# Kernel tuning notes

Measured on AMD Instinct MI355X. Metric: run time of the kernel, lower is better.

Reference implementation:

```python
import jax, jax.numpy as jnp
from jax import lax
import numpy as np

EPS = 1e-5  # BatchNorm2d default eps

def _cbs(x, w, g, b, m, v, pad):
    # Conv2d(bias=False) + BatchNorm2d (eval mode, running stats) + SiLU
    y = lax.conv_general_dilated(x, w, (1, 1), [(pad, pad), (pad, pad)],
                                 dimension_numbers=('NCHW', 'OIHW', 'NCHW'))
    y = (y - m[None, :, None, None]) * (g / jnp.sqrt(v + EPS))[None, :, None, None] + b[None, :, None, None]
    return y * jax.nn.sigmoid(y)

def setup_inputs():
    key = jax.random.key(0)
    B, C1, C2, H, W = 2, 128, 128, 20, 20
    ks = iter(jax.random.split(key, 16))
    def wconv(o, i, s):
        return jax.random.normal(next(ks), (o, i, s, s), jnp.float32) / np.float32(np.sqrt(i * s * s))
    def bn(cdim):
        k1, k2 = jax.random.split(next(ks))
        g = jax.random.uniform(k1, (cdim,), jnp.float32, 0.5, 1.5)
        b = jax.random.normal(k2, (cdim,), jnp.float32) * 0.1
        return g, b, jnp.zeros((cdim,), jnp.float32), jnp.ones((cdim,), jnp.float32)
    inp = {'x': jax.random.normal(next(ks), (B, C1, H, W), jnp.float32)}
    inp['w1'] = wconv(C2, C1, 1); inp['g1'], inp['b1'], inp['m1'], inp['v1'] = bn(C2)
    inp['w2'] = wconv(C2, C1, 1); inp['g2'], inp['b2'], inp['m2'], inp['v2'] = bn(C2)
    inp['wr1'] = wconv(C2, 2 * C2, 1); inp['gr1'], inp['br1'], inp['mr1'], inp['vr1'] = bn(C2)
    inp['wr2'] = wconv(C2, C2, 3); inp['gr2'], inp['br2'], inp['mr2'], inp['vr2'] = bn(C2)
    inp['wr3'] = wconv(1, C2, 1); inp['gr3'], inp['br3'], inp['mr3'], inp['vr3'] = bn(1)
    return inp

def reference(x, w1, g1, b1, m1, v1, w2, g2, b2, m2, v2,
              wr1, gr1, br1, mr1, vr1, wr2, gr2, br2, mr2, vr2,
              wr3, gr3, br3, mr3, vr3):
    B, C, H, W = x.shape
    HW = H * W
    # feat: [B, HW, C2]
    feat = _cbs(x, w1, g1, b1, m1, v1, 0).reshape(B, -1, HW).transpose(0, 2, 1)
    C2 = feat.shape[-1]
    # pairwise concat: rel[b,i,j] = [feat[b,i], feat[b,j]]  -> [B, HW, HW, 2*C2]
    fi = jnp.broadcast_to(feat[:, :, None, :], (B, HW, HW, C2))
    fj = jnp.broadcast_to(feat[:, None, :, :], (B, HW, HW, C2))
    rel = jnp.concatenate([fi, fj], axis=-1)
    # faithful permute(0,3,1,2) + contiguous view to [B*HW, 2*C2, H, W]
    rel = rel.transpose(0, 3, 1, 2).reshape(B * HW, 2 * C2, H, W)
    r = _cbs(rel, wr1, gr1, br1, mr1, vr1, 0)
    r = _cbs(r, wr2, gr2, br2, mr2, vr2, 1)
    r = _cbs(r, wr3, gr3, br3, mr3, vr3, 0)  # [B*HW, 1, H, W]
    scores = r.reshape(B, HW, HW)
    # bmm aggregation then back to [B, C2, H, W]
    att = jnp.einsum('bij,bjc->bic', scores, feat).transpose(0, 2, 1).reshape(B, C2, H, W)
    return _cbs(att, w2, g2, b2, m2, v2, 0) + x
```

## Files before the change

kernel.cpp:

```cpp
#include <hip/hip_runtime.h>

#define EPS 1e-5f

typedef __bf16 bf16x8 __attribute__((ext_vector_type(8)));
typedef float  f32x4  __attribute__((ext_vector_type(4)));

__device__ __forceinline__ unsigned short f2bf(float f) {
  unsigned int u = __float_as_uint(f);
  unsigned int r = (u + 0x7fffu + ((u >> 16) & 1u)) >> 16;
  return (unsigned short)r;
}
__device__ __forceinline__ float silu(float y) {
  return y * __builtin_amdgcn_rcpf(1.f + __expf(-y));
}

__global__ void prep_kernel(const float* __restrict__ x, const float* __restrict__ w1,
                            const float* __restrict__ g1, const float* __restrict__ b1,
                            const float* __restrict__ m1, const float* __restrict__ v1,
                            const float* __restrict__ wr2, const float* __restrict__ wr1,
                            const float* __restrict__ w2,
                            float* __restrict__ feat, float* __restrict__ featT,
                            float* __restrict__ attz,
                            unsigned short* __restrict__ Apack, float* __restrict__ Pfx,
                            float* __restrict__ Wt, float* __restrict__ W2t,
                            float* __restrict__ wr1T) {
  int blk = blockIdx.x;
  int tid = threadIdx.x;
  if (blk < 400) {
    int hp = tid >> 7, c = tid & 127;
    int pp = blk * 2 + hp;
    int b = pp / 400, p = pp % 400;
    __shared__ float xv[2][128];
    xv[hp][c] = x[(b * 128 + c) * 400 + p];
    __syncthreads();
    const float4* w4 = (const float4*)(w1 + c * 128);
    const float4* v4 = (const float4*)xv[hp];
    float s0 = 0.f, s1 = 0.f, s2 = 0.f, s3 = 0.f;
#pragma unroll
    for (int i = 0; i < 32; ++i) {
      float4 wv = w4[i], xx = v4[i];
      s0 += wv.x * xx.x; s1 += wv.y * xx.y; s2 += wv.z * xx.z; s3 += wv.w * xx.w;
    }
    float s = (s0 + s1) + (s2 + s3);
    float sc = g1[c] * rsqrtf(v1[c] + EPS);
    float y = s * sc + (b1[c] - m1[c] * sc);
    float f = silu(y);
    feat[(b * 400 + p) * 128 + c] = f;
    featT[(b * 128 + c) * 400 + p] = f;
    if (p >= 200) attz[(b * 400 + p) * 128 + c] = 0.f;
  } else if (blk < 472) {
    int f = (blk - 400) * 4 + (tid >> 6);
    int lane = tid & 63;
    int tap = f >> 5, ks = (f >> 3) & 3, m8 = f & 7;
    int o  = m8 * 16 + (lane & 15);
    int cb = ks * 32 + (lane >> 4) * 8;
    unsigned short* dst = Apack + ((size_t)f * 64 + lane) * 8;
#pragma unroll
    for (int j = 0; j < 8; ++j)
      dst[j] = f2bf(wr2[(o * 128 + (cb + j)) * 9 + tap]);
  } else if (blk < 504) {
    int o = (blk - 472) * 4 + (tid >> 6);
    int lane = tid & 63;
    float4 wv = ((const float4*)(wr1 + o * 256))[lane];
    float p0 = wv.x, p1 = p0 + wv.y, p2 = p1 + wv.z, p3 = p2 + wv.w;
    float v = p3;
#pragma unroll
    for (int d = 1; d < 64; d <<= 1) {
      float t = __shfl_up(v, d);
      if (lane >= d) v += t;
    }
    float off = v - p3;
    float* Po = Pfx + o * 257;
    if (lane == 0) Po[0] = 0.f;
    Po[lane * 4 + 1] = off + p0;
    Po[lane * 4 + 2] = off + p1;
    Po[lane * 4 + 3] = off + p2;
    Po[lane * 4 + 4] = off + p3;
  } else if (blk < 648) {
    int base = (blk - 504) * 1024;
#pragma unroll
    for (int k = 0; k < 4; ++k) {
      int idx = base + k * 256 + tid;
      int tap = idx >> 14;
      int r = idx & 16383;
      int i = r >> 7, o = r & 127;
      Wt[idx] = wr2[(o * 128 + i) * 9 + tap];
    }
  } else if (blk < 712) {
    int idx = (blk - 648) * 256 + tid;
    int i = idx >> 7, o = idx & 127;
    W2t[idx] = w2[o * 128 + i];
  } else {
    int base = (blk - 712) * 1024;
#pragma unroll
    for (int k = 0; k < 4; ++k) {
      int idx = base + k * 256 + tid;
      int i = idx >> 7, o = idx & 127;
      wr1T[idx] = wr1[o * 256 + i];
    }
  }
}

__global__ __launch_bounds__(512, 4) void rel_kernel(
    const float* __restrict__ feat, const float* __restrict__ featT,
    const float* __restrict__ wr1T, const float* __restrict__ Pfx,
    const float* __restrict__ gr1, const float* __restrict__ br1,
    const float* __restrict__ mr1, const float* __restrict__ vr1,
    const unsigned short* __restrict__ Apack, const float* __restrict__ Wt,
    const float* __restrict__ gr2, const float* __restrict__ br2,
    const float* __restrict__ mr2, const float* __restrict__ vr2,
    const float* __restrict__ wr3,
    const float* __restrict__ gr3, const float* __restrict__ br3,
    const float* __restrict__ mr3, const float* __restrict__ vr3,
    float* __restrict__ att) {

  __shared__ __align__(16) unsigned short r1f[16 * 221 * 8];
  __shared__ float f0s[220], f1s[220], scoreS[208];
  __shared__ float wB0s[128], wB1s[128];
  __shared__ float sc1[128], sh1[128], sc2[128], sh2[128], w3c[128];
  __shared__ float attT[128];
  __shared__ float fA[256], r1c[128], AvS[128];
  __shared__ float vS[9 * 128];
  __shared__ float spS[9];
  __shared__ float spP[400];

  int tid = threadIdx.x, lane = tid & 63, wid = tid >> 6;
  int blk = blockIdx.x;

  if (tid < 128) {
    float s1 = gr1[tid] * rsqrtf(vr1[tid] + EPS); sc1[tid] = s1; sh1[tid] = br1[tid] - mr1[tid] * s1;
    float s2 = gr2[tid] * rsqrtf(vr2[tid] + EPS); sc2[tid] = s2; sh2[tid] = br2[tid] - mr2[tid] * s2;
    w3c[tid] = wr3[tid];
    attT[tid] = 0.f; AvS[tid] = 0.f;
  }
  float s3 = gr3[0] * rsqrtf(vr3[0] + EPS);
  float sh3 = br3[0] - mr3[0] * s3;

  if (blk < 800) {
    int idx = blk >> 1, half = blk & 1;
    int b = idx / 200, q = 200 + idx % 200;
    int c0 = (q * 256) / 400, c1 = c0 + 1;
    if (tid < 128) {
      const float* Po = Pfx + tid * 257;
      int e0 = min(256, 400 * c0 + 400 - 256 * q);
      wB0s[tid] = Po[e0];
      float wv = 0.f;
      if (c1 < 256) {
        int s1i = min(256, max(0, 400 * c1 - 256 * q));
        wv = Po[256] - Po[s1i];
      }
      wB1s[tid] = wv;
    }
    if (tid < 220) {
      int p = tid + 180 * half;
      f0s[tid] = featT[(b * 128 + (c0 - 128)) * 400 + p];
      f1s[tid] = (c1 < 256) ? featT[(b * 128 + (c1 - 128)) * 400 + p] : 0.f;
    }
    if (tid < 208) scoreS[tid] = 0.f;
    __syncthreads();

    for (int i = tid; i < 3520; i += 512) {
      int plane = i / 220, p = i - plane * 220;
      int cb = (plane >> 2) * 32 + (plane & 3) * 8;
      float fa0 = f0s[p], fa1 = f1s[p];
      unsigned int pk[4];
#pragma unroll
      for (int jp = 0; jp < 4; ++jp) {
        int c = cb + jp * 2;
        float y0 = wB0s[c] * fa0 + wB1s[c] * fa1;     y0 = y0 * sc1[c] + sh1[c];
        float y1 = wB0s[c + 1] * fa0 + wB1s[c + 1] * fa1; y1 = y1 * sc1[c + 1] + sh1[c + 1];
        pk[jp] = (unsigned int)f2bf(silu(y0)) | ((unsigned int)f2bf(silu(y1)) << 16);
      }
      *(uint4*)&r1f[(plane * 221 + p) * 8] = make_uint4(pk[0], pk[1], pk[2], pk[3]);
    }
    if (tid < 16) *(uint4*)&r1f[(tid * 221 + 220) * 8] = make_uint4(0, 0, 0, 0);

    int wm = wid & 1, wn = wid >> 1;
    int ntcnt = (wn == 0) ? 4 : 3;
    int n16 = lane & 15, quad = lane >> 4;
    int hA[4], wA[4], poA[4]; bool pov[4];
#pragma unroll
    for (int t = 0; t < 4; ++t) {
      int po = (wn + 4 * t) * 16 + n16;
      poA[t] = po; pov[t] = po < 200;
      int pg = half * 200 + po;
      hA[t] = pg / 20; wA[t] = pg - 20 * hA[t];
    }
    f32x4 acc[4][4];
#pragma unroll
    for (int mt = 0; mt < 4; ++mt)
#pragma unroll
      for (int t = 0; t < 4; ++t) acc[mt][t] = f32x4{0.f, 0.f, 0.f, 0.f};

    __syncthreads();

    const char* wbase = (const char*)Apack + (size_t)((wm * 4) * 64 + lane) * 16;
    for (int tap = 0; tap < 9; ++tap) {
      int dy = tap / 3 - 1, dx = tap % 3 - 1;
      int pp[4];
#pragma unroll
      for (int t = 0; t < 4; ++t) {
        int hh = hA[t] + dy, ww = wA[t] + dx;
        bool valid = pov[t] & (hh >= 0) & (hh < 20) & (ww >= 0) & (ww < 20);
        pp[t] = valid ? (hh - 9 * half) * 20 + ww : 220;
      }
#pragma unroll
      for (int ks = 0; ks < 4; ++ks) {
        const char* wp = wbase + (size_t)(tap * 4 + ks) * 8192;
        bf16x8 af0 = *(const bf16x8*)(wp);
        bf16x8 af1 = *(const bf16x8*)(wp + 1024);
        bf16x8 af2 = *(const bf16x8*)(wp + 2048);
        bf16x8 af3 = *(const bf16x8*)(wp + 3072);
        int pbase = (ks * 4 + quad) * 221;
#pragma unroll
        for (int t = 0; t < 4; ++t) {
          if (t < ntcnt) {
            bf16x8 bfr = *(const bf16x8*)&r1f[(pbase + pp[t]) * 8];
            acc[0][t] = __builtin_amdgcn_mfma_f32_16x16x32_bf16(af0, bfr, acc[0][t], 0, 0, 0);
            acc[1][t] = __builtin_amdgcn_mfma_f32_16x16x32_bf16(af1, bfr, acc[1][t], 0, 0, 0);
            acc[2][t] = __builtin_amdgcn_mfma_f32_16x16x32_bf16(af2, bfr, acc[2][t], 0, 0, 0);
            acc[3][t] = __builtin_amdgcn_mfma_f32_16x16x32_bf16(af3, bfr, acc[3][t], 0, 0, 0);
          }
        }
      }
    }

#pragma unroll
    for (int t = 0; t < 4; ++t) {
      if (t < ntcnt) {
        float ps = 0.f;
#pragma unroll
        for (int mt = 0; mt < 4; ++mt) {
#pragma unroll
          for (int r = 0; r < 4; ++r) {
            int o = wm * 64 + mt * 16 + quad * 4 + r;
            float y = acc[mt][t][r] * sc2[o] + sh2[o];
            ps += silu(y) * w3c[o];
          }
        }
        ps += __shfl_xor(ps, 16);
        ps += __shfl_xor(ps, 32);
        if (quad == 0 && pov[t]) atomicAdd(&scoreS[poA[t]], ps);
      }
    }
    __syncthreads();

    if (tid < 200) scoreS[tid] = silu(scoreS[tid] * s3 + sh3);
    __syncthreads();

    {
      int c = tid & 127, part = tid >> 7;
      float s = 0.f;
      int j0 = part * 50;
      for (int j = j0; j < j0 + 50; ++j)
        s += scoreS[j] * feat[(b * 400 + half * 200 + j) * 128 + c];
      atomicAdd(&attT[c], s);
    }
    __syncthreads();
    if (tid < 128)
      atomicAdd(&att[((size_t)(b * 400 + q)) * 128 + tid], attT[tid]);
  } else {
    int cidx = blk - 800;
    int b = cidx / 200, q = cidx % 200;
    if (tid < 256) {
      int u = q * 256 + tid; int c = u / 400, i2 = u - c * 400;
      fA[tid] = featT[(b * 128 + c) * 400 + i2];
    }
    for (int k = tid; k < 1152; k += 512) vS[k] = 0.f;
    __syncthreads();
    {
      int o = tid & 127, part = tid >> 7;
      const float* wt = wr1T + part * 64 * 128 + o;
      const float* fv = fA + part * 64;
      float a = 0.f;
#pragma unroll 8
      for (int k = 0; k < 64; ++k) a += wt[k * 128] * fv[k];
      atomicAdd(&AvS[o], a);
    }
    __syncthreads();
    if (tid < 128) r1c[tid] = silu(AvS[tid] * sc1[tid] + sh1[tid]);
    __syncthreads();
    {
      int o = tid & 127, part = tid >> 7;
      const float* rc = r1c + part * 32;
      for (int tap = 0; tap < 9; ++tap) {
        const float* wt = Wt + tap * 16384 + part * 32 * 128 + o;
        float s = 0.f;
#pragma unroll 8
        for (int i2 = 0; i2 < 32; ++i2) s += wt[i2 * 128] * rc[i2];
        atomicAdd(&vS[tap * 128 + o], s);
      }
    }
    __syncthreads();
    for (int pat = wid; pat < 9; pat += 8) {
      int ry = pat / 3, rx = pat % 3;
      float ps = 0.f;
      for (int oo = lane; oo < 128; oo += 64) {
        float y = 0.f;
#pragma unroll
        for (int dy = -1; dy <= 1; ++dy) {
          if ((ry == 0 && dy < 0) || (ry == 2 && dy > 0)) continue;
#pragma unroll
          for (int dx = -1; dx <= 1; ++dx) {
            if ((rx == 0 && dx < 0) || (rx == 2 && dx > 0)) continue;
            y += vS[((dy + 1) * 3 + (dx + 1)) * 128 + oo];
          }
        }
        y = y * sc2[oo] + sh2[oo];
        ps += silu(y) * w3c[oo];
      }
#pragma unroll
      for (int sft = 32; sft >= 1; sft >>= 1) ps += __shfl_xor(ps, sft);
      if (lane == 0) spS[pat] = silu(ps * s3 + sh3);
    }
    __syncthreads();

    for (int p = tid; p < 400; p += 512) {
      int r = p / 20, cm = p - 20 * r;
      int ry = (r == 0) ? 0 : (r == 19) ? 2 : 1;
      int rx = (cm == 0) ? 0 : (cm == 19) ? 2 : 1;
      spP[p] = spS[ry * 3 + rx];
    }
    __syncthreads();
    {
      int c = tid & 127, part = tid >> 7;
      const float* fb = feat + ((size_t)(b * 400) + part * 100) * 128 + c;
      const float* sp = spP + part * 100;
      float s = 0.f;
      for (int j = 0; j < 100; ++j) s += sp[j] * fb[(size_t)j * 128];
      atomicAdd(&attT[c], s);
    }
    __syncthreads();
    if (tid < 128)
      att[((size_t)(b * 400 + q)) * 128 + tid] = attT[tid];
  }
}

__global__ void out_kernel(const float* __restrict__ att, const float* __restrict__ x,
                           const float* __restrict__ w2,
                           const float* __restrict__ g2, const float* __restrict__ b2,
                           const float* __restrict__ m2, const float* __restrict__ v2,
                           float* __restrict__ out) {
  int pp = blockIdx.x;
  int b = pp / 400, p = pp % 400;
  int tid = threadIdx.x;
  __shared__ float av[128];
  if (tid < 128) av[tid] = att[(size_t)(b * 400 + p) * 128 + tid];
  __syncthreads();
  int c = tid >> 1, part = tid & 1;
  const float4* w4 = (const float4*)(w2 + c * 128 + part * 64);
  const float4* v4 = (const float4*)(av + part * 64);
  float s0 = 0.f, s1 = 0.f, s2 = 0.f, s3 = 0.f;
#pragma unroll
  for (int i = 0; i < 16; ++i) {
    float4 wv = w4[i], xx = v4[i];
    s0 += wv.x * xx.x; s1 += wv.y * xx.y; s2 += wv.z * xx.z; s3 += wv.w * xx.w;
  }
  float s = (s0 + s1) + (s2 + s3);
  s += __shfl_xor(s, 1);
  if (part == 0) {
    float sc = g2[c] * rsqrtf(v2[c] + EPS);
    float y = s * sc + (b2[c] - m2[c] * sc);
    int xi = (b * 128 + c) * 400 + p;
    out[xi] = silu(y) + x[xi];
  }
}

extern "C" void kernel_launch(void* const* d_in, const int* in_sizes, int n_in,
                              void* d_out, int out_size, void* d_ws, size_t ws_size,
                              hipStream_t stream) {
  const float* x   = (const float*)d_in[0];
  const float* w1  = (const float*)d_in[1];
  const float* g1  = (const float*)d_in[2];
  const float* b1  = (const float*)d_in[3];
  const float* m1  = (const float*)d_in[4];
  const float* v1  = (const float*)d_in[5];
  const float* w2  = (const float*)d_in[6];
  const float* g2  = (const float*)d_in[7];
  const float* b2  = (const float*)d_in[8];
  const float* m2  = (const float*)d_in[9];
  const float* v2  = (const float*)d_in[10];
  const float* wr1 = (const float*)d_in[11];
  const float* gr1 = (const float*)d_in[12];
  const float* br1 = (const float*)d_in[13];
  const float* mr1 = (const float*)d_in[14];
  const float* vr1 = (const float*)d_in[15];
  const float* wr2 = (const float*)d_in[16];
  const float* gr2 = (const float*)d_in[17];
  const float* br2 = (const float*)d_in[18];
  const float* mr2 = (const float*)d_in[19];
  const float* vr2 = (const float*)d_in[20];
  const float* wr3 = (const float*)d_in[21];
  const float* gr3 = (const float*)d_in[22];
  const float* br3 = (const float*)d_in[23];
  const float* mr3 = (const float*)d_in[24];
  const float* vr3 = (const float*)d_in[25];
  float* out = (float*)d_out;

  char* ws = (char*)d_ws;
  float*          feat  = (float*)ws;
  float*          attb  = (float*)(ws + 409600);
  unsigned short* Apack = (unsigned short*)(ws + 819200);
  float*          Pfx   = (float*)(ws + 1114112);
  float*          Wt    = (float*)(ws + 1245696);
  float*          W2t   = (float*)(ws + 1835520);
  float*          featT = (float*)(ws + 1901056);
  float*          wr1T  = (float*)(ws + 2310656);

  prep_kernel<<<744, 256, 0, stream>>>(x, w1, g1, b1, m1, v1, wr2, wr1, w2,
                                       feat, featT, attb, Apack, Pfx, Wt, W2t, wr1T);
  rel_kernel<<<1200, 512, 0, stream>>>(feat, featT, wr1T, Pfx, gr1, br1, mr1, vr1,
                                       Apack, Wt,
                                       gr2, br2, mr2, vr2, wr3, gr3, br3, mr3, vr3, attb);
  out_kernel<<<800, 256, 0, stream>>>(attb, x, w2, g2, b2, m2, v2, out);
}
```

Measured before the change: 204.2 us.

## Drop weight transpose prep and read raw weights with vectorized loads in rel_kernel

Removes the prep-kernel blocks that transposed wr1, wr2 and w2 into workspace buffers. The compact-path blocks in rel_kernel now read the original row-major weights with float4 loads, split the reduction across 4 lanes and combine with shuffles instead of shared-memory atomics. Block indices are interleaved so every third block is a compact block, mixing the two workloads across the grid. Some dot-product loops are also unrolled; the new reads of wr2 with a 9-stride pattern are less coalesced per lane.

```diff
diff --git a/kernel.cpp b/kernel.cpp
--- a/kernel.cpp
+++ b/kernel.cpp
@@ -18,12 +18,9 @@
                             const float* __restrict__ g1, const float* __restrict__ b1,
                             const float* __restrict__ m1, const float* __restrict__ v1,
                             const float* __restrict__ wr2, const float* __restrict__ wr1,
-                            const float* __restrict__ w2,
                             float* __restrict__ feat, float* __restrict__ featT,
                             float* __restrict__ attz,
-                            unsigned short* __restrict__ Apack, float* __restrict__ Pfx,
-                            float* __restrict__ Wt, float* __restrict__ W2t,
-                            float* __restrict__ wr1T) {
+                            unsigned short* __restrict__ Apack, float* __restrict__ Pfx) {
   int blk = blockIdx.x;
   int tid = threadIdx.x;
   if (blk < 400) {
@@ -58,7 +55,7 @@
 #pragma unroll
     for (int j = 0; j < 8; ++j)
       dst[j] = f2bf(wr2[(o * 128 + (cb + j)) * 9 + tap]);
-  } else if (blk < 504) {
+  } else {
     int o = (blk - 472) * 4 + (tid >> 6);
     int lane = tid & 63;
     float4 wv = ((const float4*)(wr1 + o * 256))[lane];
@@ -76,37 +73,15 @@
     Po[lane * 4 + 2] = off + p1;
     Po[lane * 4 + 3] = off + p2;
     Po[lane * 4 + 4] = off + p3;
-  } else if (blk < 648) {
-    int base = (blk - 504) * 1024;
-#pragma unroll
-    for (int k = 0; k < 4; ++k) {
-      int idx = base + k * 256 + tid;
-      int tap = idx >> 14;
-      int r = idx & 16383;
-      int i = r >> 7, o = r & 127;
-      Wt[idx] = wr2[(o * 128 + i) * 9 + tap];
-    }
-  } else if (blk < 712) {
-    int idx = (blk - 648) * 256 + tid;
-    int i = idx >> 7, o = idx & 127;
-    W2t[idx] = w2[o * 128 + i];
-  } else {
-    int base = (blk - 712) * 1024;
-#pragma unroll
-    for (int k = 0; k < 4; ++k) {
-      int idx = base + k * 256 + tid;
-      int i = idx >> 7, o = idx & 127;
-      wr1T[idx] = wr1[o * 256 + i];
-    }
   }
 }
 
 __global__ __launch_bounds__(512, 4) void rel_kernel(
     const float* __restrict__ feat, const float* __restrict__ featT,
-    const float* __restrict__ wr1T, const float* __restrict__ Pfx,
+    const float* __restrict__ wr1, const float* __restrict__ Pfx,
     const float* __restrict__ gr1, const float* __restrict__ br1,
     const float* __restrict__ mr1, const float* __restrict__ vr1,
-    const unsigned short* __restrict__ Apack, const float* __restrict__ Wt,
+    const unsigned short* __restrict__ Apack, const float* __restrict__ wr2,
     const float* __restrict__ gr2, const float* __restrict__ br2,
     const float* __restrict__ mr2, const float* __restrict__ vr2,
     const float* __restrict__ wr3,
@@ -119,25 +94,28 @@
   __shared__ float wB0s[128], wB1s[128];
   __shared__ float sc1[128], sh1[128], sc2[128], sh2[128], w3c[128];
   __shared__ float attT[128];
-  __shared__ float fA[256], r1c[128], AvS[128];
+  __shared__ __align__(16) float fA[256];
+  __shared__ float r1c[128], AvS[128];
   __shared__ float vS[9 * 128];
   __shared__ float spS[9];
   __shared__ float spP[400];
 
   int tid = threadIdx.x, lane = tid & 63, wid = tid >> 6;
   int blk = blockIdx.x;
+  int g3 = blk / 3, r3 = blk - g3 * 3;
 
   if (tid < 128) {
     float s1 = gr1[tid] * rsqrtf(vr1[tid] + EPS); sc1[tid] = s1; sh1[tid] = br1[tid] - mr1[tid] * s1;
     float s2 = gr2[tid] * rsqrtf(vr2[tid] + EPS); sc2[tid] = s2; sh2[tid] = br2[tid] - mr2[tid] * s2;
     w3c[tid] = wr3[tid];
-    attT[tid] = 0.f; AvS[tid] = 0.f;
+    attT[tid] = 0.f;
   }
   float s3 = gr3[0] * rsqrtf(vr3[0] + EPS);
   float sh3 = br3[0] - mr3[0] * s3;
 
-  if (blk < 800) {
-    int idx = blk >> 1, half = blk & 1;
+  if (r3 < 2) {
+    int mainId = g3 * 2 + r3;
+    int idx = mainId >> 1, half = mainId & 1;
     int b = idx / 200, q = 200 + idx % 200;
     int c0 = (q * 256) / 400, c1 = c0 + 1;
     if (tid < 128) {
@@ -252,43 +230,68 @@
       int c = tid & 127, part = tid >> 7;
       float s = 0.f;
       int j0 = part * 50;
-      for (int j = j0; j < j0 + 50; ++j)
-        s += scoreS[j] * feat[(b * 400 + half * 200 + j) * 128 + c];
+      const float* fb = feat + ((size_t)(b * 400 + half * 200 + j0)) * 128 + c;
+#pragma unroll 10
+      for (int j = 0; j < 50; ++j)
+        s += scoreS[j0 + j] * fb[(size_t)j * 128];
       atomicAdd(&attT[c], s);
     }
     __syncthreads();
     if (tid < 128)
       atomicAdd(&att[((size_t)(b * 400 + q)) * 128 + tid], attT[tid]);
   } else {
-    int cidx = blk - 800;
-    int b = cidx / 200, q = cidx % 200;
+    int b = g3 / 200, q = g3 - (g3 / 200) * 200;
     if (tid < 256) {
       int u = q * 256 + tid; int c = u / 400, i2 = u - c * 400;
       fA[tid] = featT[(b * 128 + c) * 400 + i2];
     }
-    for (int k = tid; k < 1152; k += 512) vS[k] = 0.f;
     __syncthreads();
     {
-      int o = tid & 127, part = tid >> 7;
-      const float* wt = wr1T + part * 64 * 128 + o;
-      const float* fv = fA + part * 64;
-      float a = 0.f;
-#pragma unroll 8
-      for (int k = 0; k < 64; ++k) a += wt[k * 128] * fv[k];
-      atomicAdd(&AvS[o], a);
+      int o = tid >> 2, kq = tid & 3;
+      const float4* w4 = (const float4*)(wr1 + (size_t)o * 256 + kq * 64);
+      const float4* f4p = (const float4*)(fA + kq * 64);
+      float s0 = 0.f, s1 = 0.f, s2 = 0.f, s3v = 0.f;
+#pragma unroll
+      for (int j = 0; j < 16; ++j) {
+        float4 wv = w4[j], xv = f4p[j];
+        s0 += wv.x * xv.x; s1 += wv.y * xv.y; s2 += wv.z * xv.z; s3v += wv.w * xv.w;
+      }
+      float s = (s0 + s1) + (s2 + s3v);
+      s += __shfl_xor(s, 1);
+      s += __shfl_xor(s, 2);
+      if (kq == 0) AvS[o] = s;
     }
     __syncthreads();
     if (tid < 128) r1c[tid] = silu(AvS[tid] * sc1[tid] + sh1[tid]);
     __syncthreads();
     {
-      int o = tid & 127, part = tid >> 7;
-      const float* rc = r1c + part * 32;
-      for (int tap = 0; tap < 9; ++tap) {
-        const float* wt = Wt + tap * 16384 + part * 32 * 128 + o;
-        float s = 0.f;
-#pragma unroll 8
-        for (int i2 = 0; i2 < 32; ++i2) s += wt[i2 * 128] * rc[i2];
-        atomicAdd(&vS[tap * 128 + o], s);
+      int o = tid >> 2, part = tid & 3;
+      const float4* wp4 = (const float4*)(wr2 + (size_t)(o * 128 + part * 32) * 9);
+      const float* rcb = r1c + part * 32;
+      float s[9];
+#pragma unroll
+      for (int t9 = 0; t9 < 9; ++t9) s[t9] = 0.f;
+      for (int gch = 0; gch < 8; ++gch) {
+        float rca[4];
+#pragma unroll
+        for (int j = 0; j < 4; ++j) rca[j] = rcb[gch * 4 + j];
+        const float4* wg = wp4 + gch * 9;
+#pragma unroll
+        for (int j = 0; j < 9; ++j) {
+          float4 wv = wg[j];
+          int e0 = 4 * j;
+          s[(e0 + 0) % 9] += wv.x * rca[(e0 + 0) / 9];
+          s[(e0 + 1) % 9] += wv.y * rca[(e0 + 1) / 9];
+          s[(e0 + 2) % 9] += wv.z * rca[(e0 + 2) / 9];
+          s[(e0 + 3) % 9] += wv.w * rca[(e0 + 3) / 9];
+        }
+      }
+#pragma unroll
+      for (int t9 = 0; t9 < 9; ++t9) {
+        float v = s[t9];
+        v += __shfl_xor(v, 1);
+        v += __shfl_xor(v, 2);
+        if (part == 0) vS[t9 * 128 + o] = v;
       }
     }
     __syncthreads();
@@ -327,6 +330,7 @@
       const float* fb = feat + ((size_t)(b * 400) + part * 100) * 128 + c;
       const float* sp = spP + part * 100;
       float s = 0.f;
+#pragma unroll 10
       for (int j = 0; j < 100; ++j) s += sp[j] * fb[(size_t)j * 128];
       atomicAdd(&attT[c], s);
     }
@@ -402,15 +406,12 @@
   float*          attb  = (float*)(ws + 409600);
   unsigned short* Apack = (unsigned short*)(ws + 819200);
   float*          Pfx   = (float*)(ws + 1114112);
-  float*          Wt    = (float*)(ws + 1245696);
-  float*          W2t   = (float*)(ws + 1835520);
   float*          featT = (float*)(ws + 1901056);
-  float*          wr1T  = (float*)(ws + 2310656);
-
-  prep_kernel<<<744, 256, 0, stream>>>(x, w1, g1, b1, m1, v1, wr2, wr1, w2,
-                                       feat, featT, attb, Apack, Pfx, Wt, W2t, wr1T);
-  rel_kernel<<<1200, 512, 0, stream>>>(feat, featT, wr1T, Pfx, gr1, br1, mr1, vr1,
-                                       Apack, Wt,
+
+  prep_kernel<<<504, 256, 0, stream>>>(x, w1, g1, b1, m1, v1, wr2, wr1,
+                                       feat, featT, attb, Apack, Pfx);
+  rel_kernel<<<1200, 512, 0, stream>>>(feat, featT, wr1, Pfx, gr1, br1, mr1, vr1,
+                                       Apack, wr2,
                                        gr2, br2, mr2, vr2, wr3, gr3, br3, mr3, vr3, attb);
   out_kernel<<<800, 256, 0, stream>>>(attb, x, w2, g2, b2, m2, v2, out);
 }
```

New measurement: 354.8 us. +73.8%, slower.
